# Optimization experiments

Hardware: AMD Instinct MI355X
Metric: run time of the kernel (lower is better)

Reference implementation:

```python
import jax, jax.numpy as jnp
import numpy as np

N_QUBITS = 10
N_LAYERS = 3
TWO_PI = np.float32(2.0 * np.pi)


def _apply_1q(state, m, wire, n):
    """Apply 2x2 unitary m to qubit `wire` (wire 0 = MSB) of state [B, 2^n]."""
    B = state.shape[0]
    st = state.reshape(B, 2 ** wire, 2, 2 ** (n - wire - 1))
    st = jnp.einsum('pq,bxqy->bxpy', m, st)
    return st.reshape(B, -1)


def _rot(angles):
    # PennyLane Rot(phi, theta, omega) = RZ(omega) @ RY(theta) @ RZ(phi)
    phi, theta, omega = angles[0], angles[1], angles[2]
    c = jnp.cos(theta / 2)
    s = jnp.sin(theta / 2)
    ep = jnp.exp(-0.5j * (phi + omega))
    em = jnp.exp(-0.5j * (phi - omega))
    return jnp.stack([jnp.stack([ep * c, -jnp.conj(em) * s]),
                      jnp.stack([em * s, jnp.conj(ep) * c])])


def _rot_layer(state, w, n):
    # StronglyEntanglingLayers single-layer Rot block: one Rot per wire. w: [n, 3]
    for j in range(n):
        state = _apply_1q(state, _rot(w[j]), j, n)
    return state


def _circuit(x, weights1, weights2):
    n = N_QUBITS
    B = x.shape[0]
    dim = 2 ** n
    idx = jnp.arange(dim)
    # bits[k, j]: value of qubit j in basis state k (wire 0 = MSB)
    bits = ((idx[:, None] >> (n - 1 - jnp.arange(n)[None, :])) & 1).astype(jnp.float32)
    signs = 1.0 - 2.0 * bits                       # eigenvalues of Z per wire, [dim, n]
    # ring of CZ entanglers (range-1, layer index 0): CZ(i, (i+1) % n) for all i
    pair = bits * jnp.roll(bits, -1, axis=1)
    cz = (1.0 - 2.0 * (jnp.sum(pair, axis=1) % 2.0))  # diagonal, [dim]

    state = jnp.zeros((B, dim), jnp.complex64).at[:, 0].set(1.0)

    for l in range(N_LAYERS):
        state = _rot_layer(state, weights1[l, 0], n)   # StronglyEntanglingLayers Rot block
        state = state * cz[None, :]                    # CZ ring (diagonal)
        # data re-uploading: RZ(x_j) on wire j, all wires fused into one diagonal phase
        state = state * jnp.exp(-0.5j * (x @ signs.T))
    state = _rot_layer(state, weights2[0], n)          # final entangling layer
    state = state * cz[None, :]

    probs = state.real ** 2 + state.imag ** 2          # [B, dim]
    return probs @ signs                               # <Z_j> per wire, [B, n]


def setup_inputs() -> dict:
    key = jax.random.key(0)
    k1, k2, k3 = jax.random.split(key, 3)
    x = jax.random.uniform(k1, (2048, N_QUBITS), jnp.float32) * TWO_PI
    weights1 = jax.random.uniform(k2, (N_LAYERS, 1, N_QUBITS, 3), jnp.float32) * TWO_PI
    weights2 = jax.random.uniform(k3, (1, N_QUBITS, 3), jnp.float32) * TWO_PI
    return {"x": x, "weights1": weights1, "weights2": weights2}


def reference(x, weights1, weights2):
    return _circuit(x, weights1, weights2)
```

## Files before the change

kernel.cpp:

```cpp
#include <hip/hip_runtime.h>
#include <math.h>

#define NQ 10

typedef float v2f __attribute__((ext_vector_type(2)));

static __device__ __forceinline__ v2f mk2(float a, float b) { v2f r; r.x = a; r.y = b; return r; }
static __device__ __forceinline__ v2f sp2(float a)          { v2f r; r.x = a; r.y = a; return r; }
static __device__ __forceinline__ v2f pkfma(v2f a, v2f b, v2f c) { return __builtin_elementwise_fma(a, b, c); }

template<int MSK>
static __device__ __forceinline__ float lxor(float v) {
    if constexpr (MSK == 1) {
        const int s = __float_as_int(v);
        return __int_as_float(__builtin_amdgcn_update_dpp(s, s, 0xB1, 0xF, 0xF, false));
    } else if constexpr (MSK == 2) {
        const int s = __float_as_int(v);
        return __int_as_float(__builtin_amdgcn_update_dpp(s, s, 0x4E, 0xF, 0xF, false));
    } else if constexpr (MSK == 4) {
        const int s = __float_as_int(v);
        int t = __builtin_amdgcn_update_dpp(s, s, 0x104, 0xF, 0x5, false);
        t     = __builtin_amdgcn_update_dpp(t, s, 0x114, 0xF, 0xA, false);
        return __int_as_float(t);
    } else if constexpr (MSK == 8) {
        const int s = __float_as_int(v);
        return __int_as_float(__builtin_amdgcn_update_dpp(s, s, 0x128, 0xF, 0xF, false));
    } else if constexpr (MSK == 16) {
        return __int_as_float(__builtin_amdgcn_ds_swizzle(__float_as_int(v), 0x401F));
    } else {
        return __shfl_xor(v, 32, 64);
    }
}
template<int MSK>
static __device__ __forceinline__ v2f lxor2(v2f v) { return mk2(lxor<MSK>(v.x), lxor<MSK>(v.y)); }

#define PLS32(a, b) asm("v_permlane32_swap_b32 %0, %1" : "+v"(a), "+v"(b))
#define PLS16(a, b) asm("v_permlane16_swap_b32 %0, %1" : "+v"(a), "+v"(b))

__global__ __launch_bounds__(256, 2) void qlayer_kernel(
    const float* __restrict__ x,
    const float* __restrict__ w1,
    const float* __restrict__ w2,
    float* __restrict__ out)
{
    __shared__ float ry[4 * 20];
    __shared__ float au[3 * 10];

    const int t    = threadIdx.x;
    const int lane = t & 63;
    const int w    = t >> 6;
    const int b    = __builtin_amdgcn_readfirstlane((blockIdx.x << 2) + w);

    if (t < 40) {
        const int L = t / 10, j = t - L * 10;
        const float th = (L < 3) ? w1[L * 30 + j * 3 + 1] : w2[j * 3 + 1];
        float c, s;
        __sincosf(0.5f * th, &s, &c);
        ry[L * 20 + j * 2 + 0] = c;
        ry[L * 20 + j * 2 + 1] = s;
    } else if (t >= 64 && t < 94) {
        const int i = t - 64, L = i / 10, j = i - L * 10;
        au[i] = w1[L * 30 + j * 3 + 2] + ((L < 2) ? w1[(L + 1) * 30 + j * 3] : w2[j * 3]);
    }

    float xv[NQ];
#pragma unroll
    for (int j = 0; j < NQ; ++j) xv[j] = x[b * NQ + j];

    int msk[4];
#pragma unroll
    for (int p = 0; p < 4; ++p) msk[p] = ((lane >> p) & 1) ? 0 : 0x80000000;

    float czm[16];
#pragma unroll
    for (int m = 0; m < 16; ++m) {
        const int k  = (m << 6) | lane;
        const int kr = ((k << 1) | (k >> 9)) & 1023;
        czm[m] = (__popc(k & kr) & 1) ? -1.f : 1.f;
    }

    __syncthreads();

    v2f dr[8], di[8];
#define BUILD_D(IDX)                                                                   \
    {                                                                                  \
        float A[NQ];                                                                   \
        _Pragma("unroll")                                                              \
        for (int j = 0; j < NQ; ++j) A[j] = au[(IDX) * 10 + j] + xv[j];                \
        float SA = 0.f;                                                                \
        _Pragma("unroll")                                                              \
        for (int j = 0; j < NQ; ++j) SA += A[j];                                       \
        float Tl = 0.f;                                                                \
        _Pragma("unroll")                                                              \
        for (int p = 0; p < 6; ++p) Tl += ((lane >> p) & 1) ? A[9 - p] : 0.f;          \
        const float base = -0.5f * SA + Tl;                                            \
        float fr[4], fi[4];                                                            \
        _Pragma("unroll")                                                              \
        for (int q = 0; q < 4; ++q) __sincosf(A[3 - q], &fi[q], &fr[q]);               \
        float dmr[16], dmi[16];                                                        \
        __sincosf(base, &dmi[0], &dmr[0]);                                             \
        _Pragma("unroll")                                                              \
        for (int m = 1; m < 16; ++m) {                                                 \
            const int q  = (m & 1) ? 0 : (m & 2) ? 1 : (m & 4) ? 2 : 3;                \
            const int pm = m & (m - 1);                                                \
            dmr[m] = dmr[pm] * fr[q] - dmi[pm] * fi[q];                                \
            dmi[m] = dmr[pm] * fi[q] + dmi[pm] * fr[q];                                \
        }                                                                              \
        _Pragma("unroll")                                                              \
        for (int p = 0; p < 8; ++p) {                                                  \
            dr[p] = mk2(dmr[2*p] * czm[2*p], dmr[2*p+1] * czm[2*p+1]);                 \
            di[p] = mk2(dmi[2*p] * czm[2*p], dmi[2*p+1] * czm[2*p+1]);                 \
        }                                                                              \
    }

    float Plo = 1.f;
#pragma unroll
    for (int p = 0; p < 6; ++p) {
        const float cc = ry[(9 - p) * 2], ss = ry[(9 - p) * 2 + 1];
        Plo *= ((lane >> p) & 1) ? ss : cc;
    }
    float Pm[16];
    {
        const float c0 = ry[0], s0 = ry[1], c1 = ry[2], s1 = ry[3];
        const float c2 = ry[4], s2 = ry[5], c3 = ry[6], s3 = ry[7];
        float P2[2] = {c3, s3};
        float P4[4], P8[8];
#pragma unroll
        for (int m = 0; m < 4; ++m)  P4[m] = ((m >> 1) ? s2 : c2) * P2[m & 1];
#pragma unroll
        for (int m = 0; m < 8; ++m)  P8[m] = ((m >> 2) ? s1 : c1) * P4[m & 3];
#pragma unroll
        for (int m = 0; m < 16; ++m) Pm[m] = ((m >> 3) ? s0 : c0) * P8[m & 7];
    }

    BUILD_D(0)
    v2f sr[8], si[8];
#pragma unroll
    for (int p = 0; p < 8; ++p) {
        const v2f pv = sp2(Plo) * mk2(Pm[2 * p], Pm[2 * p + 1]);
        sr[p] = pv * dr[p];
        si[p] = pv * di[p];
    }

#define RY_LANE_S(J, MSK)                                                       \
    {                                                                           \
        const float c = rl[(J) * 2], s = rl[(J) * 2 + 1];                       \
        const float ssg = __int_as_float(__float_as_int(s) ^ msk[9 - (J)]);     \
        _Pragma("unroll")                                                       \
        for (int p = 0; p < 8; ++p) {                                           \
            const float qx = lxor<MSK>(sr[p].x);                                \
            const float qy = lxor<MSK>(sr[p].y);                                \
            const float rx = lxor<MSK>(si[p].x);                                \
            const float ryv = lxor<MSK>(si[p].y);                               \
            sr[p].x = fmaf(qx,  ssg, c * sr[p].x);                              \
            sr[p].y = fmaf(qy,  ssg, c * sr[p].y);                              \
            si[p].x = fmaf(rx,  ssg, c * si[p].x);                              \
            si[p].y = fmaf(ryv, ssg, c * si[p].y);                              \
        }                                                                       \
    }

#define RY_LANE_V(J, MSK)                                                       \
    {                                                                           \
        const float c = rl[(J) * 2], s = rl[(J) * 2 + 1];                       \
        const float ssg = __int_as_float(__float_as_int(s) ^ msk[9 - (J)]);     \
        const v2f C = sp2(c), S = sp2(ssg);                                     \
        _Pragma("unroll")                                                       \
        for (int p = 0; p < 8; ++p) {                                           \
            const v2f qr = lxor2<MSK>(sr[p]);                                   \
            const v2f qi = lxor2<MSK>(si[p]);                                   \
            sr[p] = pkfma(C, sr[p], S * qr);                                    \
            si[p] = pkfma(C, si[p], S * qi);                                    \
        }                                                                       \
    }

#define RY_PLPAIR(J, PLS)                                                       \
    {                                                                           \
        const float c = rl[(J) * 2], s = rl[(J) * 2 + 1];                       \
        const v2f C = sp2(c), S = sp2(s), nS = sp2(-s);                         \
        _Pragma("unroll")                                                       \
        for (int p = 0; p < 8; ++p) {                                           \
            float ux = sr[p].x, uy = sr[p].y;                                   \
            float vx = si[p].x, vy = si[p].y;                                   \
            PLS(ux, vx); PLS(uy, vy);                                           \
            const v2f u = mk2(ux, uy), v = mk2(vx, vy);                         \
            const v2f t1 = pkfma(C, u, nS * v);                                 \
            const v2f t2 = pkfma(C, v,  S * u);                                 \
            float ax = t1.x, ay = t1.y, bx = t2.x, by = t2.y;                   \
            PLS(ax, bx); PLS(ay, by);                                           \
            sr[p] = mk2(ax, ay); si[p] = mk2(bx, by);                           \
        }                                                                       \
    }

#pragma unroll
    for (int L = 1; L <= 3; ++L) {
        const float* rl = ry + L * 20;

        RY_PLPAIR(4, PLS32)
        RY_PLPAIR(5, PLS16)
        RY_LANE_S(6, 8)
        RY_LANE_V(7, 4)
        RY_LANE_S(8, 2)
        RY_LANE_S(9, 1)

#pragma unroll
        for (int j = 0; j < 3; ++j) {
            const int pb = 4 >> j;
            const float c = rl[j * 2], s = rl[j * 2 + 1];
            const v2f C = sp2(c), S = sp2(s), nS = sp2(-s);
#pragma unroll
            for (int p0 = 0; p0 < 8; ++p0) {
                if (p0 & pb) continue;
                const int p1 = p0 | pb;
                const v2f a0r = sr[p0], a1r = sr[p1];
                const v2f a0i = si[p0], a1i = si[p1];
                sr[p0] = pkfma(C, a0r, nS * a1r);
                sr[p1] = pkfma(C, a1r,  S * a0r);
                si[p0] = pkfma(C, a0i, nS * a1i);
                si[p1] = pkfma(C, a1i,  S * a0i);
            }
        }

        {
            const float c = rl[6], s = rl[7];
            const v2f C = sp2(c), Sw = mk2(-s, s);
#pragma unroll
            for (int p = 0; p < 8; ++p) {
                const v2f swr = mk2(sr[p].y, sr[p].x);
                const v2f swi = mk2(si[p].y, si[p].x);
                sr[p] = pkfma(C, sr[p], Sw * swr);
                si[p] = pkfma(C, si[p], Sw * swi);
            }
        }

        if (L < 3) {
            BUILD_D(L)
#pragma unroll
            for (int p = 0; p < 8; ++p) {
                const v2f tr = pkfma(sr[p], dr[p], -(si[p] * di[p]));
                si[p] = pkfma(sr[p], di[p], si[p] * dr[p]);
                sr[p] = tr;
            }
        }
    }
#undef RY_LANE_S
#undef RY_LANE_V
#undef RY_PLPAIR
#undef BUILD_D

    float pe[8], po[8];
#pragma unroll
    for (int p = 0; p < 8; ++p) {
        const v2f pk = pkfma(sr[p], sr[p], si[p] * si[p]);
        pe[p] = pk.x + pk.y;
        po[p] = pk.x - pk.y;
    }
    float tot = 0.f, t0 = 0.f, t1 = 0.f, t2 = 0.f, t3 = 0.f;
#pragma unroll
    for (int p = 0; p < 8; ++p) {
        tot += pe[p];
        t0  += (p & 4) ? -pe[p] : pe[p];
        t1  += (p & 2) ? -pe[p] : pe[p];
        t2  += (p & 1) ? -pe[p] : pe[p];
        t3  += po[p];
    }
    v2f u01 = mk2(t0, t1), u23 = mk2(t2, t3);
    u01 += lxor2<1>(u01);  u23 += lxor2<1>(u23);
    u01 += lxor2<2>(u01);  u23 += lxor2<2>(u23);
    u01 += lxor2<4>(u01);  u23 += lxor2<4>(u23);
    u01 += lxor2<8>(u01);  u23 += lxor2<8>(u23);
    u01 += lxor2<16>(u01); u23 += lxor2<16>(u23);
    u01 += lxor2<32>(u01); u23 += lxor2<32>(u23);

    float Sa = tot, T, D0, D1, D2, D3, D4, D5;
    T = lxor<1>(Sa);  D0 = Sa - T; Sa += T;
    T = lxor<2>(Sa);  D1 = Sa - T; Sa += T;
    T = lxor<4>(Sa);  D2 = Sa - T; Sa += T;
    T = lxor<8>(Sa);  D3 = Sa - T; Sa += T;
    T = lxor<16>(Sa); D4 = Sa - T; Sa += T;
    T = lxor<32>(Sa); D5 = Sa - T;
    D0 += lxor<2>(D0); D0 += lxor<4>(D0); D0 += lxor<8>(D0); D0 += lxor<16>(D0); D0 += lxor<32>(D0);
    D1 += lxor<4>(D1); D1 += lxor<8>(D1); D1 += lxor<16>(D1); D1 += lxor<32>(D1);
    D2 += lxor<8>(D2); D2 += lxor<16>(D2); D2 += lxor<32>(D2);
    D3 += lxor<16>(D3); D3 += lxor<32>(D3);
    D4 += lxor<32>(D4);

    if (lane == 0) {
        float* o = out + b * NQ;
        o[0] = u01.x; o[1] = u01.y; o[2] = u23.x; o[3] = u23.y;
        o[4] = D5;    o[5] = D4;    o[6] = D3;    o[7] = D2;    o[8] = D1;    o[9] = D0;
    }
}

extern "C" void kernel_launch(void* const* d_in, const int* in_sizes, int n_in,
                              void* d_out, int out_size, void* d_ws, size_t ws_size,
                              hipStream_t stream) {
    const float* x  = (const float*)d_in[0];
    const float* w1 = (const float*)d_in[1];
    const float* w2 = (const float*)d_in[2];
    float* out = (float*)d_out;
    const int B = in_sizes[0] / NQ;
    qlayer_kernel<<<B / 4, 256, 0, stream>>>(x, w1, w2, out);
}
```

Measured before the change: 17.81 us.

## Process two batch elements per wavefront to amortize setup and increase ILP

Each wavefront now simulates two batch samples interleaved, which halves the grid and doubles the register state per thread. Per-block setup (shared rotation tables, CZ masks, RY products) is amortized over twice the work, and the interleaved gate loops expose more independent instructions to hide DPP/permlane latency. The layer loop is no longer unrolled, and launch bounds drop to one block per CU-slot to allow the larger register footprint. In exchange, occupancy falls and only 256 blocks are launched for the batch of 2048, so fewer CUs may be used and latency hiding relies on the in-thread parallelism.

```diff
diff --git a/kernel.cpp b/kernel.cpp
--- a/kernel.cpp
+++ b/kernel.cpp
@@ -37,7 +37,7 @@
 #define PLS32(a, b) asm("v_permlane32_swap_b32 %0, %1" : "+v"(a), "+v"(b))
 #define PLS16(a, b) asm("v_permlane16_swap_b32 %0, %1" : "+v"(a), "+v"(b))
 
-__global__ __launch_bounds__(256, 2) void qlayer_kernel(
+__global__ __launch_bounds__(256, 1) void qlayer_kernel(
     const float* __restrict__ x,
     const float* __restrict__ w1,
     const float* __restrict__ w2,
@@ -49,7 +49,7 @@
     const int t    = threadIdx.x;
     const int lane = t & 63;
     const int w    = t >> 6;
-    const int b    = __builtin_amdgcn_readfirstlane((blockIdx.x << 2) + w);
+    const int b0   = (blockIdx.x << 3) + (w << 1);
 
     if (t < 40) {
         const int L = t / 10, j = t - L * 10;
@@ -63,9 +63,17 @@
         au[i] = w1[L * 30 + j * 3 + 2] + ((L < 2) ? w1[(L + 1) * 30 + j * 3] : w2[j * 3]);
     }
 
-    float xv[NQ];
-#pragma unroll
-    for (int j = 0; j < NQ; ++j) xv[j] = x[b * NQ + j];
+    float xv[2][NQ];
+    {
+        const float4* xp = (const float4*)(x + b0 * NQ);
+        const float4 q0 = xp[0], q1 = xp[1], q2 = xp[2], q3 = xp[3], q4 = xp[4];
+        xv[0][0] = q0.x; xv[0][1] = q0.y; xv[0][2] = q0.z; xv[0][3] = q0.w;
+        xv[0][4] = q1.x; xv[0][5] = q1.y; xv[0][6] = q1.z; xv[0][7] = q1.w;
+        xv[0][8] = q2.x; xv[0][9] = q2.y;
+        xv[1][0] = q2.z; xv[1][1] = q2.w; xv[1][2] = q3.x; xv[1][3] = q3.y;
+        xv[1][4] = q3.z; xv[1][5] = q3.w; xv[1][6] = q4.x; xv[1][7] = q4.y;
+        xv[1][8] = q4.z; xv[1][9] = q4.w;
+    }
 
     int msk[4];
 #pragma unroll
@@ -81,12 +89,12 @@
 
     __syncthreads();
 
-    v2f dr[8], di[8];
-#define BUILD_D(IDX)                                                                   \
+    v2f dr[2][8], di[2][8];
+#define BUILD_D(IDX, E)                                                                \
     {                                                                                  \
         float A[NQ];                                                                   \
         _Pragma("unroll")                                                              \
-        for (int j = 0; j < NQ; ++j) A[j] = au[(IDX) * 10 + j] + xv[j];                \
+        for (int j = 0; j < NQ; ++j) A[j] = au[(IDX) * 10 + j] + xv[E][j];             \
         float SA = 0.f;                                                                \
         _Pragma("unroll")                                                              \
         for (int j = 0; j < NQ; ++j) SA += A[j];                                       \
@@ -108,8 +116,8 @@
         }                                                                              \
         _Pragma("unroll")                                                              \
         for (int p = 0; p < 8; ++p) {                                                  \
-            dr[p] = mk2(dmr[2*p] * czm[2*p], dmr[2*p+1] * czm[2*p+1]);                 \
-            di[p] = mk2(dmi[2*p] * czm[2*p], dmi[2*p+1] * czm[2*p+1]);                 \
+            dr[E][p] = mk2(dmr[2*p] * czm[2*p], dmr[2*p+1] * czm[2*p+1]);              \
+            di[E][p] = mk2(dmi[2*p] * czm[2*p], dmi[2*p+1] * czm[2*p+1]);              \
         }                                                                              \
     }
 
@@ -133,13 +141,14 @@
         for (int m = 0; m < 16; ++m) Pm[m] = ((m >> 3) ? s0 : c0) * P8[m & 7];
     }
 
-    BUILD_D(0)
-    v2f sr[8], si[8];
+    BUILD_D(0, 0)
+    BUILD_D(0, 1)
+    v2f sr[2][8], si[2][8];
 #pragma unroll
     for (int p = 0; p < 8; ++p) {
         const v2f pv = sp2(Plo) * mk2(Pm[2 * p], Pm[2 * p + 1]);
-        sr[p] = pv * dr[p];
-        si[p] = pv * di[p];
+        sr[0][p] = pv * dr[0][p];  si[0][p] = pv * di[0][p];
+        sr[1][p] = pv * dr[1][p];  si[1][p] = pv * di[1][p];
     }
 
 #define RY_LANE_S(J, MSK)                                                       \
@@ -147,15 +156,18 @@
         const float c = rl[(J) * 2], s = rl[(J) * 2 + 1];                       \
         const float ssg = __int_as_float(__float_as_int(s) ^ msk[9 - (J)]);     \
         _Pragma("unroll")                                                       \
-        for (int p = 0; p < 8; ++p) {                                           \
-            const float qx = lxor<MSK>(sr[p].x);                                \
-            const float qy = lxor<MSK>(sr[p].y);                                \
-            const float rx = lxor<MSK>(si[p].x);                                \
-            const float ryv = lxor<MSK>(si[p].y);                               \
-            sr[p].x = fmaf(qx,  ssg, c * sr[p].x);                              \
-            sr[p].y = fmaf(qy,  ssg, c * sr[p].y);                              \
-            si[p].x = fmaf(rx,  ssg, c * si[p].x);                              \
-            si[p].y = fmaf(ryv, ssg, c * si[p].y);                              \
+        for (int e = 0; e < 2; ++e) {                                           \
+            _Pragma("unroll")                                                   \
+            for (int p = 0; p < 8; ++p) {                                       \
+                const float qx  = lxor<MSK>(sr[e][p].x);                        \
+                const float qy  = lxor<MSK>(sr[e][p].y);                        \
+                const float rx  = lxor<MSK>(si[e][p].x);                        \
+                const float ryv = lxor<MSK>(si[e][p].y);                        \
+                sr[e][p].x = fmaf(qx,  ssg, c * sr[e][p].x);                    \
+                sr[e][p].y = fmaf(qy,  ssg, c * sr[e][p].y);                    \
+                si[e][p].x = fmaf(rx,  ssg, c * si[e][p].x);                    \
+                si[e][p].y = fmaf(ryv, ssg, c * si[e][p].y);                    \
+            }                                                                   \
         }                                                                       \
     }
 
@@ -165,11 +177,14 @@
         const float ssg = __int_as_float(__float_as_int(s) ^ msk[9 - (J)]);     \
         const v2f C = sp2(c), S = sp2(ssg);                                     \
         _Pragma("unroll")                                                       \
-        for (int p = 0; p < 8; ++p) {                                           \
-            const v2f qr = lxor2<MSK>(sr[p]);                                   \
-            const v2f qi = lxor2<MSK>(si[p]);                                   \
-            sr[p] = pkfma(C, sr[p], S * qr);                                    \
-            si[p] = pkfma(C, si[p], S * qi);                                    \
+        for (int e = 0; e < 2; ++e) {                                           \
+            _Pragma("unroll")                                                   \
+            for (int p = 0; p < 8; ++p) {                                       \
+                const v2f qr = lxor2<MSK>(sr[e][p]);                            \
+                const v2f qi = lxor2<MSK>(si[e][p]);                            \
+                sr[e][p] = pkfma(C, sr[e][p], S * qr);                          \
+                si[e][p] = pkfma(C, si[e][p], S * qi);                          \
+            }                                                                   \
         }                                                                       \
     }
 
@@ -178,20 +193,23 @@
         const float c = rl[(J) * 2], s = rl[(J) * 2 + 1];                       \
         const v2f C = sp2(c), S = sp2(s), nS = sp2(-s);                         \
         _Pragma("unroll")                                                       \
-        for (int p = 0; p < 8; ++p) {                                           \
-            float ux = sr[p].x, uy = sr[p].y;                                   \
-            float vx = si[p].x, vy = si[p].y;                                   \
-            PLS(ux, vx); PLS(uy, vy);                                           \
-            const v2f u = mk2(ux, uy), v = mk2(vx, vy);                         \
-            const v2f t1 = pkfma(C, u, nS * v);                                 \
-            const v2f t2 = pkfma(C, v,  S * u);                                 \
-            float ax = t1.x, ay = t1.y, bx = t2.x, by = t2.y;                   \
-            PLS(ax, bx); PLS(ay, by);                                           \
-            sr[p] = mk2(ax, ay); si[p] = mk2(bx, by);                           \
+        for (int e = 0; e < 2; ++e) {                                           \
+            _Pragma("unroll")                                                   \
+            for (int p = 0; p < 8; ++p) {                                       \
+                float ux = sr[e][p].x, uy = sr[e][p].y;                         \
+                float vx = si[e][p].x, vy = si[e][p].y;                         \
+                PLS(ux, vx); PLS(uy, vy);                                       \
+                const v2f u = mk2(ux, uy), v = mk2(vx, vy);                     \
+                const v2f t1 = pkfma(C, u, nS * v);                             \
+                const v2f t2 = pkfma(C, v,  S * u);                             \
+                float ax = t1.x, ay = t1.y, bx = t2.x, by = t2.y;               \
+                PLS(ax, bx); PLS(ay, by);                                       \
+                sr[e][p] = mk2(ax, ay); si[e][p] = mk2(bx, by);                 \
+            }                                                                   \
         }                                                                       \
     }
 
-#pragma unroll
+#pragma unroll 1
     for (int L = 1; L <= 3; ++L) {
         const float* rl = ry + L * 20;
 
@@ -208,15 +226,18 @@
             const float c = rl[j * 2], s = rl[j * 2 + 1];
             const v2f C = sp2(c), S = sp2(s), nS = sp2(-s);
 #pragma unroll
-            for (int p0 = 0; p0 < 8; ++p0) {
-                if (p0 & pb) continue;
-                const int p1 = p0 | pb;
-                const v2f a0r = sr[p0], a1r = sr[p1];
-                const v2f a0i = si[p0], a1i = si[p1];
-                sr[p0] = pkfma(C, a0r, nS * a1r);
-                sr[p1] = pkfma(C, a1r,  S * a0r);
-                si[p0] = pkfma(C, a0i, nS * a1i);
-                si[p1] = pkfma(C, a1i,  S * a0i);
+            for (int e = 0; e < 2; ++e) {
+#pragma unroll
+                for (int p0 = 0; p0 < 8; ++p0) {
+                    if (p0 & pb) continue;
+                    const int p1 = p0 | pb;
+                    const v2f a0r = sr[e][p0], a1r = sr[e][p1];
+                    const v2f a0i = si[e][p0], a1i = si[e][p1];
+                    sr[e][p0] = pkfma(C, a0r, nS * a1r);
+                    sr[e][p1] = pkfma(C, a1r,  S * a0r);
+                    si[e][p0] = pkfma(C, a0i, nS * a1i);
+                    si[e][p1] = pkfma(C, a1i,  S * a0i);
+                }
             }
         }
 
@@ -224,21 +245,28 @@
             const float c = rl[6], s = rl[7];
             const v2f C = sp2(c), Sw = mk2(-s, s);
 #pragma unroll
-            for (int p = 0; p < 8; ++p) {
-                const v2f swr = mk2(sr[p].y, sr[p].x);
-                const v2f swi = mk2(si[p].y, si[p].x);
-                sr[p] = pkfma(C, sr[p], Sw * swr);
-                si[p] = pkfma(C, si[p], Sw * swi);
+            for (int e = 0; e < 2; ++e) {
+#pragma unroll
+                for (int p = 0; p < 8; ++p) {
+                    const v2f swr = mk2(sr[e][p].y, sr[e][p].x);
+                    const v2f swi = mk2(si[e][p].y, si[e][p].x);
+                    sr[e][p] = pkfma(C, sr[e][p], Sw * swr);
+                    si[e][p] = pkfma(C, si[e][p], Sw * swi);
+                }
             }
         }
 
         if (L < 3) {
-            BUILD_D(L)
-#pragma unroll
-            for (int p = 0; p < 8; ++p) {
-                const v2f tr = pkfma(sr[p], dr[p], -(si[p] * di[p]));
-                si[p] = pkfma(sr[p], di[p], si[p] * dr[p]);
-                sr[p] = tr;
+            BUILD_D(L, 0)
+            BUILD_D(L, 1)
+#pragma unroll
+            for (int e = 0; e < 2; ++e) {
+#pragma unroll
+                for (int p = 0; p < 8; ++p) {
+                    const v2f tr = pkfma(sr[e][p], dr[e][p], -(si[e][p] * di[e][p]));
+                    si[e][p] = pkfma(sr[e][p], di[e][p], si[e][p] * dr[e][p]);
+                    sr[e][p] = tr;
+                }
             }
         }
     }
@@ -247,47 +275,50 @@
 #undef RY_PLPAIR
 #undef BUILD_D
 
-    float pe[8], po[8];
-#pragma unroll
-    for (int p = 0; p < 8; ++p) {
-        const v2f pk = pkfma(sr[p], sr[p], si[p] * si[p]);
-        pe[p] = pk.x + pk.y;
-        po[p] = pk.x - pk.y;
-    }
-    float tot = 0.f, t0 = 0.f, t1 = 0.f, t2 = 0.f, t3 = 0.f;
-#pragma unroll
-    for (int p = 0; p < 8; ++p) {
-        tot += pe[p];
-        t0  += (p & 4) ? -pe[p] : pe[p];
-        t1  += (p & 2) ? -pe[p] : pe[p];
-        t2  += (p & 1) ? -pe[p] : pe[p];
-        t3  += po[p];
-    }
-    v2f u01 = mk2(t0, t1), u23 = mk2(t2, t3);
-    u01 += lxor2<1>(u01);  u23 += lxor2<1>(u23);
-    u01 += lxor2<2>(u01);  u23 += lxor2<2>(u23);
-    u01 += lxor2<4>(u01);  u23 += lxor2<4>(u23);
-    u01 += lxor2<8>(u01);  u23 += lxor2<8>(u23);
-    u01 += lxor2<16>(u01); u23 += lxor2<16>(u23);
-    u01 += lxor2<32>(u01); u23 += lxor2<32>(u23);
-
-    float Sa = tot, T, D0, D1, D2, D3, D4, D5;
-    T = lxor<1>(Sa);  D0 = Sa - T; Sa += T;
-    T = lxor<2>(Sa);  D1 = Sa - T; Sa += T;
-    T = lxor<4>(Sa);  D2 = Sa - T; Sa += T;
-    T = lxor<8>(Sa);  D3 = Sa - T; Sa += T;
-    T = lxor<16>(Sa); D4 = Sa - T; Sa += T;
-    T = lxor<32>(Sa); D5 = Sa - T;
-    D0 += lxor<2>(D0); D0 += lxor<4>(D0); D0 += lxor<8>(D0); D0 += lxor<16>(D0); D0 += lxor<32>(D0);
-    D1 += lxor<4>(D1); D1 += lxor<8>(D1); D1 += lxor<16>(D1); D1 += lxor<32>(D1);
-    D2 += lxor<8>(D2); D2 += lxor<16>(D2); D2 += lxor<32>(D2);
-    D3 += lxor<16>(D3); D3 += lxor<32>(D3);
-    D4 += lxor<32>(D4);
-
-    if (lane == 0) {
-        float* o = out + b * NQ;
-        o[0] = u01.x; o[1] = u01.y; o[2] = u23.x; o[3] = u23.y;
-        o[4] = D5;    o[5] = D4;    o[6] = D3;    o[7] = D2;    o[8] = D1;    o[9] = D0;
+#pragma unroll
+    for (int e = 0; e < 2; ++e) {
+        float pe[8], po[8];
+#pragma unroll
+        for (int p = 0; p < 8; ++p) {
+            const v2f pk = pkfma(sr[e][p], sr[e][p], si[e][p] * si[e][p]);
+            pe[p] = pk.x + pk.y;
+            po[p] = pk.x - pk.y;
+        }
+        float tot = 0.f, t0 = 0.f, t1 = 0.f, t2 = 0.f, t3 = 0.f;
+#pragma unroll
+        for (int p = 0; p < 8; ++p) {
+            tot += pe[p];
+            t0  += (p & 4) ? -pe[p] : pe[p];
+            t1  += (p & 2) ? -pe[p] : pe[p];
+            t2  += (p & 1) ? -pe[p] : pe[p];
+            t3  += po[p];
+        }
+        v2f u01 = mk2(t0, t1), u23 = mk2(t2, t3);
+        u01 += lxor2<1>(u01);  u23 += lxor2<1>(u23);
+        u01 += lxor2<2>(u01);  u23 += lxor2<2>(u23);
+        u01 += lxor2<4>(u01);  u23 += lxor2<4>(u23);
+        u01 += lxor2<8>(u01);  u23 += lxor2<8>(u23);
+        u01 += lxor2<16>(u01); u23 += lxor2<16>(u23);
+        u01 += lxor2<32>(u01); u23 += lxor2<32>(u23);
+
+        float Sa = tot, T, D0, D1, D2, D3, D4, D5;
+        T = lxor<1>(Sa);  D0 = Sa - T; Sa += T;
+        T = lxor<2>(Sa);  D1 = Sa - T; Sa += T;
+        T = lxor<4>(Sa);  D2 = Sa - T; Sa += T;
+        T = lxor<8>(Sa);  D3 = Sa - T; Sa += T;
+        T = lxor<16>(Sa); D4 = Sa - T; Sa += T;
+        T = lxor<32>(Sa); D5 = Sa - T;
+        D0 += lxor<2>(D0); D0 += lxor<4>(D0); D0 += lxor<8>(D0); D0 += lxor<16>(D0); D0 += lxor<32>(D0);
+        D1 += lxor<4>(D1); D1 += lxor<8>(D1); D1 += lxor<16>(D1); D1 += lxor<32>(D1);
+        D2 += lxor<8>(D2); D2 += lxor<16>(D2); D2 += lxor<32>(D2);
+        D3 += lxor<16>(D3); D3 += lxor<32>(D3);
+        D4 += lxor<32>(D4);
+
+        if (lane == 0) {
+            float* o = out + (b0 + e) * NQ;
+            o[0] = u01.x; o[1] = u01.y; o[2] = u23.x; o[3] = u23.y;
+            o[4] = D5;    o[5] = D4;    o[6] = D3;    o[7] = D2;    o[8] = D1;    o[9] = D0;
+        }
     }
 }
 
@@ -299,5 +330,5 @@
     const float* w2 = (const float*)d_in[2];
     float* out = (float*)d_out;
     const int B = in_sizes[0] / NQ;
-    qlayer_kernel<<<B / 4, 256, 0, stream>>>(x, w1, w2, out);
+    qlayer_kernel<<<B / 8, 256, 0, stream>>>(x, w1, w2, out);
 }
```

After: 18.35 us. 3.0% more time.
